# Optimization experiments

Hardware: AMD Instinct MI355X
Metric: run time of the kernel (lower is better)

Reference implementation:

```python
import jax, jax.numpy as jnp
import numpy as np
import math

B, S, E, H, DFF = 8, 1024, 1024, 16, 4096
DK = E // H
EPS = 1e-6


def _layernorm(x, alpha, bias):
    # Faithful to the torch module: uses unbiased std (ddof=1) and divides by (std + eps)
    mean = jnp.mean(x, axis=-1, keepdims=True)
    var = jnp.sum((x - mean) ** 2, axis=-1, keepdims=True) / (x.shape[-1] - 1)
    std = jnp.sqrt(var)
    return alpha * (x - mean) / (std + EPS) + bias


def setup_inputs() -> dict:
    key = jax.random.key(0)
    ks = jax.random.split(key, 16)
    sc_e = 1.0 / math.sqrt(E)
    sc_f = 1.0 / math.sqrt(DFF)
    inp = {
        "x": jax.random.normal(ks[0], (B, S, E), dtype=jnp.float32),
        "mask": jnp.ones((1, 1, S, S), dtype=jnp.int32),
        # linear weights stored as (in, out)
        "wq": jax.random.normal(ks[1], (E, E), jnp.float32) * sc_e,
        "bq": jnp.zeros((E,), jnp.float32),
        "wk": jax.random.normal(ks[2], (E, E), jnp.float32) * sc_e,
        "bk": jnp.zeros((E,), jnp.float32),
        "wv": jax.random.normal(ks[3], (E, E), jnp.float32) * sc_e,
        "bv": jnp.zeros((E,), jnp.float32),
        "wo": jax.random.normal(ks[4], (E, E), jnp.float32) * sc_e,
        "bo": jnp.zeros((E,), jnp.float32),
        "w1": jax.random.normal(ks[5], (E, DFF), jnp.float32) * sc_e,
        "b1": jnp.zeros((DFF,), jnp.float32),
        "w2": jax.random.normal(ks[6], (DFF, E), jnp.float32) * sc_f,
        "b2": jnp.zeros((E,), jnp.float32),
        "ln1_a": jnp.ones((E,), jnp.float32),
        "ln1_b": jnp.zeros((E,), jnp.float32),
        "ln2_a": jnp.ones((E,), jnp.float32),
        "ln2_b": jnp.zeros((E,), jnp.float32),
    }
    return inp


def _mha(x, mask, wq, bq, wk, bk, wv, bv, wo, bo):
    q = (x @ wq + bq).reshape(B, S, H, DK).transpose(0, 2, 1, 3)  # [B,H,S,DK]
    k = (x @ wk + bk).reshape(B, S, H, DK).transpose(0, 2, 1, 3)
    v = (x @ wv + bv).reshape(B, S, H, DK).transpose(0, 2, 1, 3)
    scores = jnp.einsum("bhqd,bhkd->bhqk", q, k) / math.sqrt(DK)  # [B,H,S,S]
    scores = jnp.where(mask == 0, jnp.float32(-1e9), scores)
    attn = jax.nn.softmax(scores, axis=-1)
    out = jnp.einsum("bhqk,bhkd->bhqd", attn, v)  # [B,H,S,DK]
    out = out.transpose(0, 2, 1, 3).reshape(B, S, E)
    return out @ wo + bo


def reference(x, mask, wq, bq, wk, bk, wv, bv, wo, bo, w1, b1, w2, b2,
              ln1_a, ln1_b, ln2_a, ln2_b):
    # Residual connection 1 (pre-norm): x + dropout(attn(norm(x))) ; dropout=0 at eval
    h1 = x + _mha(_layernorm(x, ln1_a, ln1_b), mask, wq, bq, wk, bk, wv, bv, wo, bo)
    # Residual connection 2: h1 + ffn(norm(h1))
    n2 = _layernorm(h1, ln2_a, ln2_b)
    ff = jax.nn.relu(n2 @ w1 + b1) @ w2 + b2
    return h1 + ff
```

## Files before the change

kernel.cpp:

```cpp
#include <hip/hip_runtime.h>
#include <hip/hip_bf16.h>
#include <cstdint>
#include <cstddef>

#define BB   8
#define SS   1024
#define EE   1024
#define HH   16
#define DKK  64
#define DFFN 4096
#define NROWS (BB*SS)

typedef __attribute__((ext_vector_type(8))) short short8;
typedef __attribute__((ext_vector_type(4))) short s16x4;
typedef __attribute__((ext_vector_type(4))) float f32x4;

__device__ __forceinline__ short f2bf(float f) {
  __hip_bfloat16 h = __float2bfloat16(f);
  return __builtin_bit_cast(short, h);
}

__device__ __forceinline__ void gload_lds16(const void* g, void* l) {
  __builtin_amdgcn_global_load_lds((const __attribute__((address_space(1))) void*)g,
                                   (__attribute__((address_space(3))) void*)l, 16, 0, 0);
}

__device__ __forceinline__ f32x4 mfma16(s16x4 a, s16x4 b, f32x4 c) {
#if __has_builtin(__builtin_amdgcn_mfma_f32_16x16x16_bf16)
  return __builtin_amdgcn_mfma_f32_16x16x16_bf16(a, b, c, 0, 0, 0);
#elif __has_builtin(__builtin_amdgcn_mfma_f32_16x16x16bf16_1k)
  return __builtin_amdgcn_mfma_f32_16x16x16bf16_1k(a, b, c, 0, 0, 0);
#else
  f32x4 d = c;
  asm("v_mfma_f32_16x16x16_bf16 %0, %1, %2, %0" : "+v"(d) : "v"(a), "v"(b));
  return d;
#endif
}

__global__ __launch_bounds__(256) void wtrans_kernel(const float* __restrict__ in,
                                                     short* __restrict__ out,
                                                     int R, int C) {
  __shared__ float tile[32][33];
  int c0 = blockIdx.x * 32, r0 = blockIdx.y * 32;
  int tx = threadIdx.x, ty = threadIdx.y;
#pragma unroll
  for (int i = 0; i < 32; i += 8)
    tile[ty + i][tx] = in[(size_t)(r0 + ty + i) * C + (c0 + tx)];
  __syncthreads();
#pragma unroll
  for (int i = 0; i < 32; i += 8)
    out[(size_t)(c0 + ty + i) * R + (r0 + tx)] = f2bf(tile[tx][ty + i]);
}

__global__ __launch_bounds__(256) void ln_kernel(const float* __restrict__ x,
                                                 const float* __restrict__ alpha,
                                                 const float* __restrict__ beta,
                                                 short* __restrict__ out) {
  __shared__ float sbuf[4];
  int row = blockIdx.x;
  int tid = threadIdx.x;
  const float* xr = x + (size_t)row * EE;
  float4 v = reinterpret_cast<const float4*>(xr)[tid];
  float s = v.x + v.y + v.z + v.w;
#pragma unroll
  for (int o = 32; o > 0; o >>= 1) s += __shfl_down(s, o);
  if ((tid & 63) == 0) sbuf[tid >> 6] = s;
  __syncthreads();
  float mean = (sbuf[0] + sbuf[1] + sbuf[2] + sbuf[3]) * (1.0f / EE);
  __syncthreads();
  float dx = v.x - mean, dy = v.y - mean, dz = v.z - mean, dw = v.w - mean;
  float sq = dx * dx + dy * dy + dz * dz + dw * dw;
#pragma unroll
  for (int o = 32; o > 0; o >>= 1) sq += __shfl_down(sq, o);
  if ((tid & 63) == 0) sbuf[tid >> 6] = sq;
  __syncthreads();
  float var = (sbuf[0] + sbuf[1] + sbuf[2] + sbuf[3]) * (1.0f / (EE - 1));
  float inv = 1.0f / (sqrtf(var) + 1e-6f);
  float4 a = reinterpret_cast<const float4*>(alpha)[tid];
  float4 b = reinterpret_cast<const float4*>(beta)[tid];
  size_t base = (size_t)row * EE + tid * 4;
  out[base + 0] = f2bf(a.x * dx * inv + b.x);
  out[base + 1] = f2bf(a.y * dy * inv + b.y);
  out[base + 2] = f2bf(a.z * dz * inv + b.z);
  out[base + 3] = f2bf(a.w * dw * inv + b.w);
}

template <int EPI>
__global__ __launch_bounds__(512, 2) void gemm256(const short* __restrict__ A,
                                                  const short* __restrict__ Bt,
                                                  const float* __restrict__ bias,
                                                  const float* __restrict__ resid,
                                                  void* __restrict__ out,
                                                  int N, int K, int NTN) {
  extern __shared__ char lds[];
  int tid = threadIdx.x, lane = tid & 63, w = tid >> 6;
  int wm = w >> 2, wn = w & 3;
  int g = lane >> 4, c = lane & 15;

  int nwg = gridDim.x, wg = blockIdx.x;
  int swg = (wg & 7) * (nwg >> 3) + (wg >> 3);
  int mt = swg / NTN, nt = swg % NTN;
  int m0 = mt * 256, n0 = nt * 256;

  int rS = tid >> 3;
  int gslot = (tid & 7) ^ ((tid >> 4) & 7);
  const short* pA = A + (size_t)(m0 + rS) * K + gslot * 8;
  const short* pB = Bt + (size_t)(n0 + rS) * K + gslot * 8;

#define STAGE_A(b, h, T)                                                                   \
  {                                                                                        \
    gload_lds16(pA + (size_t)((h)*128) * K + (size_t)(T)*64,                               \
                lds + (b)*32768 + (h)*16384 + tid * 16);                                   \
    gload_lds16(pA + (size_t)((h)*128 + 64) * K + (size_t)(T)*64,                          \
                lds + (b)*32768 + (h)*16384 + 8192 + tid * 16);                            \
  }
#define STAGE_B(b, h, T)                                                                   \
  {                                                                                        \
    gload_lds16(pB + (size_t)((h)*128) * K + (size_t)(T)*64,                               \
                lds + 65536 + (b)*32768 + (h)*16384 + tid * 16);                           \
    gload_lds16(pB + (size_t)((h)*128 + 64) * K + (size_t)(T)*64,                          \
                lds + 65536 + (b)*32768 + (h)*16384 + 8192 + tid * 16);                    \
  }
#define WAITV(NN) asm volatile("s_waitcnt vmcnt(" #NN ")" ::: "memory")

  int aoff0 = ((0 * 4 + g) ^ (c >> 1)) * 16;
  int aoff1 = ((1 * 4 + g) ^ (c >> 1)) * 16;
  char* ldsAb = lds + (wm * 128 + c) * 128;
  char* ldsBb = lds + 65536 + (wn * 64 + c) * 128;

  f32x4 acc[8][4] = {};
  short8 af[2][2], bfr[4][2];

#define READB(b)                                                                           \
  {                                                                                        \
    _Pragma("unroll") for (int nf = 0; nf < 4; ++nf) {                                     \
      bfr[nf][0] = *(const short8*)(ldsBb + (b)*32768 + nf * 2048 + aoff0);                \
      bfr[nf][1] = *(const short8*)(ldsBb + (b)*32768 + nf * 2048 + aoff1);                \
    }                                                                                      \
  }

#define PHASE(b, q, STAGEOP, ENDWAIT)                                                      \
  {                                                                                        \
    _Pragma("unroll") for (int mi = 0; mi < 2; ++mi) {                                     \
      af[mi][0] = *(const short8*)(ldsAb + (b)*32768 + ((q)*32 + mi * 16) * 128 + aoff0);  \
      af[mi][1] = *(const short8*)(ldsAb + (b)*32768 + ((q)*32 + mi * 16) * 128 + aoff1);  \
    }                                                                                      \
    STAGEOP;                                                                               \
    __builtin_amdgcn_s_barrier();                                                          \
    asm volatile("s_waitcnt lgkmcnt(0)" ::: "memory");                                     \
    __builtin_amdgcn_sched_barrier(0);                                                     \
    __builtin_amdgcn_s_setprio(1);                                                         \
    _Pragma("unroll") for (int mi = 0; mi < 2; ++mi)                                       \
      _Pragma("unroll") for (int nf = 0; nf < 4; ++nf) {                                   \
        acc[(q)*2 + mi][nf] = __builtin_amdgcn_mfma_f32_16x16x32_bf16(                     \
            af[mi][0], bfr[nf][0], acc[(q)*2 + mi][nf], 0, 0, 0);                          \
        acc[(q)*2 + mi][nf] = __builtin_amdgcn_mfma_f32_16x16x32_bf16(                     \
            af[mi][1], bfr[nf][1], acc[(q)*2 + mi][nf], 0, 0, 0);                          \
      }                                                                                    \
    __builtin_amdgcn_s_setprio(0);                                                         \
    ENDWAIT;                                                                               \
    __builtin_amdgcn_s_barrier();                                                          \
  }

  int NKT = K >> 6;

  STAGE_A(0, 0, 0); STAGE_A(0, 1, 0);
  STAGE_B(0, 0, 0); STAGE_B(0, 1, 0);
  STAGE_B(1, 0, 1); STAGE_B(1, 1, 1);
  WAITV(4);
  __builtin_amdgcn_s_barrier();

  for (int t = 0; t < NKT - 2; t += 2) {
    READB(0);
    PHASE(0, 0, STAGE_A(1, 0, t + 1), );
    PHASE(0, 1, STAGE_A(1, 1, t + 1), );
    PHASE(0, 2, STAGE_B(0, 0, t + 2), );
    PHASE(0, 3, STAGE_B(0, 1, t + 2), WAITV(4));
    READB(1);
    PHASE(1, 0, STAGE_A(0, 0, t + 2), );
    PHASE(1, 1, STAGE_A(0, 1, t + 2), );
    PHASE(1, 2, STAGE_B(1, 0, t + 3), );
    PHASE(1, 3, STAGE_B(1, 1, t + 3), WAITV(4));
  }
  {
    int t = NKT - 2;
    READB(0);
    PHASE(0, 0, STAGE_A(1, 0, t + 1), );
    PHASE(0, 1, STAGE_A(1, 1, t + 1), );
    PHASE(0, 2, , );
    PHASE(0, 3, , WAITV(0));
    READB(1);
    PHASE(1, 0, , );
    PHASE(1, 1, , );
    PHASE(1, 2, , );
    PHASE(1, 3, , );
  }

#undef STAGE_A
#undef STAGE_B
#undef READB
#undef PHASE
#undef WAITV

  int rb_ = m0 + wm * 128;
  int cb_ = n0 + wn * 64;
#pragma unroll
  for (int fm = 0; fm < 8; ++fm) {
#pragma unroll
    for (int nf = 0; nf < 4; ++nf) {
      int col = cb_ + nf * 16 + c;
      float bv = bias[col];
      if (EPI == 5) {
        int which = col >> 10;
        int inner = col & 1023;
        int h = inner >> 6, d = inner & 63;
        if (which < 2) {
          short* dst = (short*)out + (size_t)which * (8u * 1024 * 1024);
#pragma unroll
          for (int j = 0; j < 4; ++j) {
            int row = rb_ + fm * 16 + g * 4 + j;
            int b = row >> 10, s = row & 1023;
            dst[(((size_t)(b * HH + h)) * SS + s) * DKK + d] = f2bf(acc[fm][nf][j] + bv);
          }
        } else {
          int row0 = rb_ + fm * 16 + g * 4;
          int b = row0 >> 10, s0 = row0 & 1023;
          s16x4 pkv;
#pragma unroll
          for (int j = 0; j < 4; ++j) pkv[j] = f2bf(acc[fm][nf][j] + bv);
          *(s16x4*)((short*)out + 2u * 8 * 1024 * 1024 +
                    (((size_t)(b * HH + h)) * DKK + d) * SS + s0) = pkv;
        }
      } else {
#pragma unroll
        for (int j = 0; j < 4; ++j) {
          int row = rb_ + fm * 16 + g * 4 + j;
          float val = acc[fm][nf][j] + bv;
          if (EPI == 1) {
            ((short*)out)[(size_t)row * N + col] = f2bf(val > 0.f ? val : 0.f);
          } else {
            ((float*)out)[(size_t)row * N + col] = resid[(size_t)row * N + col] + val;
          }
        }
      }
    }
  }
}

__global__ __launch_bounds__(512, 1) void gemm256x128(const short* __restrict__ A,
                                                      const short* __restrict__ Bt,
                                                      const float* __restrict__ bias,
                                                      const float* __restrict__ resid,
                                                      float* __restrict__ out,
                                                      int N, int K, int NTN) {
  extern __shared__ char lds[];
  int tid = threadIdx.x, lane = tid & 63, w = tid >> 6;
  int wm = w >> 1, wn = w & 1;
  int g = lane >> 4, c = lane & 15;

  int nwg = gridDim.x, wg = blockIdx.x;
  int swg = (wg & 7) * (nwg >> 3) + (wg >> 3);
  int mt = swg / NTN, nt = swg % NTN;
  int m0 = mt * 256, n0 = nt * 128;

  int rS = tid >> 3;
  int gslot = (tid & 7) ^ ((tid >> 4) & 7);
  const short* pA = A + (size_t)(m0 + rS) * K + gslot * 8;
  const short* pB = Bt + (size_t)(n0 + rS) * K + gslot * 8;

#define STAGE_A(b, h, T)                                                                   \
  {                                                                                        \
    gload_lds16(pA + (size_t)((h)*128) * K + (size_t)(T)*64,                               \
                lds + (b)*32768 + (h)*16384 + tid * 16);                                   \
    gload_lds16(pA + (size_t)((h)*128 + 64) * K + (size_t)(T)*64,                          \
                lds + (b)*32768 + (h)*16384 + 8192 + tid * 16);                            \
  }
#define STAGE_B(b, T)                                                                      \
  {                                                                                        \
    gload_lds16(pB + (size_t)(T)*64,            lds + 65536 + (b)*16384 + tid * 16);       \
    gload_lds16(pB + (size_t)64 * K + (size_t)(T)*64,                                      \
                lds + 65536 + (b)*16384 + 8192 + tid * 16);                                \
  }
#define WAITV(NN) asm volatile("s_waitcnt vmcnt(" #NN ")" ::: "memory")

  int aoff0 = ((0 * 4 + g) ^ (c >> 1)) * 16;
  int aoff1 = ((1 * 4 + g) ^ (c >> 1)) * 16;
  char* ldsAb = lds + (wm * 64 + c) * 128;
  char* ldsBb = lds + 65536 + (wn * 64 + c) * 128;

  f32x4 acc[4][4] = {};
  short8 af[2][2], bfr[4][2];

#define READB(b)                                                                           \
  {                                                                                        \
    _Pragma("unroll") for (int nf = 0; nf < 4; ++nf) {                                     \
      bfr[nf][0] = *(const short8*)(ldsBb + (b)*16384 + nf * 2048 + aoff0);                \
      bfr[nf][1] = *(const short8*)(ldsBb + (b)*16384 + nf * 2048 + aoff1);                \
    }                                                                                      \
  }

#define PHASE(b, q, STAGEOP, ENDWAIT)                                                      \
  {                                                                                        \
    _Pragma("unroll") for (int mi = 0; mi < 2; ++mi) {                                     \
      af[mi][0] = *(const short8*)(ldsAb + (b)*32768 + ((q)*32 + mi * 16) * 128 + aoff0);  \
      af[mi][1] = *(const short8*)(ldsAb + (b)*32768 + ((q)*32 + mi * 16) * 128 + aoff1);  \
    }                                                                                      \
    STAGEOP;                                                                               \
    __builtin_amdgcn_s_barrier();                                                          \
    asm volatile("s_waitcnt lgkmcnt(0)" ::: "memory");                                     \
    __builtin_amdgcn_sched_barrier(0);                                                     \
    __builtin_amdgcn_s_setprio(1);                                                         \
    _Pragma("unroll") for (int mi = 0; mi < 2; ++mi)                                       \
      _Pragma("unroll") for (int nf = 0; nf < 4; ++nf) {                                   \
        acc[(q)*2 + mi][nf] = __builtin_amdgcn_mfma_f32_16x16x32_bf16(                     \
            af[mi][0], bfr[nf][0], acc[(q)*2 + mi][nf], 0, 0, 0);                          \
        acc[(q)*2 + mi][nf] = __builtin_amdgcn_mfma_f32_16x16x32_bf16(                     \
            af[mi][1], bfr[nf][1], acc[(q)*2 + mi][nf], 0, 0, 0);                          \
      }                                                                                    \
    __builtin_amdgcn_s_setprio(0);                                                         \
    ENDWAIT;                                                                               \
    __builtin_amdgcn_s_barrier();                                                          \
  }

  int NKT = K >> 6;

  STAGE_A(0, 0, 0); STAGE_A(0, 1, 0);
  STAGE_B(0, 0);
  STAGE_B(1, 1);
  WAITV(2);
  __builtin_amdgcn_s_barrier();

  for (int t = 0; t < NKT - 2; t += 2) {
    READB(0);
    PHASE(0, 0, STAGE_A(1, 0, t + 1); STAGE_A(1, 1, t + 1), );
    PHASE(0, 1, STAGE_B(0, t + 2), WAITV(2));
    READB(1);
    PHASE(1, 0, STAGE_A(0, 0, t + 2); STAGE_A(0, 1, t + 2), );
    PHASE(1, 1, STAGE_B(1, t + 3), WAITV(2));
  }
  READB(0);
  PHASE(0, 0, STAGE_A(1, 0, NKT - 1); STAGE_A(1, 1, NKT - 1), );
  PHASE(0, 1, , WAITV(0));
  READB(1);
  PHASE(1, 0, , );
  PHASE(1, 1, , );

#undef STAGE_A
#undef STAGE_B
#undef READB
#undef PHASE
#undef WAITV

  int rb_ = m0 + wm * 64;
  int cb_ = n0 + wn * 64;
#pragma unroll
  for (int fm = 0; fm < 4; ++fm) {
#pragma unroll
    for (int nf = 0; nf < 4; ++nf) {
      int col = cb_ + nf * 16 + c;
      float bv = bias[col];
#pragma unroll
      for (int j = 0; j < 4; ++j) {
        int row = rb_ + fm * 16 + g * 4 + j;
        out[(size_t)row * N + col] = resid[(size_t)row * N + col] + acc[fm][nf][j] + bv;
      }
    }
  }
}

__global__ __launch_bounds__(256, 3) void attn_kernel(const short* __restrict__ q,
                                                      const short* __restrict__ k,
                                                      const short* __restrict__ vt,
                                                      short* __restrict__ out) {
  __shared__ short Ks[2][64 * 64];
  __shared__ short Vs[2][64 * 64];
  int bh = blockIdx.x, qt = blockIdx.y;
  int tid = threadIdx.x, lane = tid & 63, w = tid >> 6;
  int g = lane >> 4, c = lane & 15;
  const short* qp = q + (size_t)bh * SS * DKK;
  const short* kp = k + (size_t)bh * SS * DKK;
  const short* vp = vt + (size_t)bh * DKK * SS;

  int q0 = qt * 128 + w * 32;

  short8 qf[2][2];
#pragma unroll
  for (int qb = 0; qb < 2; ++qb)
#pragma unroll
    for (int ks = 0; ks < 2; ++ks)
      qf[qb][ks] = *(const short8*)(qp + (size_t)(q0 + qb * 16 + c) * DKK + ks * 32 + g * 8);

  f32x4 oacc[2][4];
#pragma unroll
  for (int qb = 0; qb < 2; ++qb)
#pragma unroll
    for (int nd = 0; nd < 4; ++nd)
#pragma unroll
      for (int j = 0; j < 4; ++j) oacc[qb][nd][j] = 0.f;
  float mrun[2] = {-1e30f, -1e30f}, lrun[2] = {0.f, 0.f};

  int rs = lane >> 3;
  int cs = lane & 7;
  int swz = (cs ^ rs) * 8;

  int buf = 0;
#define STAGE(B, T)                                                                  \
  {                                                                                  \
    _Pragma("unroll")                                                                \
    for (int cc = 0; cc < 2; ++cc) {                                                 \
      int chunk = w * 2 + cc;                                                        \
      int row = chunk * 8 + rs;                                                      \
      gload_lds16(kp + (size_t)((T) * 64 + row) * DKK + swz, &Ks[B][chunk * 512]);   \
      gload_lds16(vp + (size_t)row * SS + (T) * 64 + swz, &Vs[B][chunk * 512]);      \
    }                                                                                \
  }

  STAGE(0, 0);
  __syncthreads();

  for (int t = 0; t < SS / 64; ++t) {
    if (t < SS / 64 - 1) STAGE(buf ^ 1, t + 1);

    f32x4 sc[2][4];
#pragma unroll
    for (int qb = 0; qb < 2; ++qb)
#pragma unroll
      for (int nf = 0; nf < 4; ++nf)
#pragma unroll
        for (int j = 0; j < 4; ++j) sc[qb][nf][j] = 0.f;
#pragma unroll
    for (int ks = 0; ks < 2; ++ks) {
      short8 kf[4];
#pragma unroll
      for (int nf = 0; nf < 4; ++nf) {
        int row = nf * 16 + c;
        int off = row * 64 + (((ks * 64 + g * 16) ^ ((c & 7) << 4)) >> 1);
        kf[nf] = *(const short8*)&Ks[buf][off];
      }
#pragma unroll
      for (int qb = 0; qb < 2; ++qb)
#pragma unroll
        for (int nf = 0; nf < 4; ++nf)
          sc[qb][nf] = __builtin_amdgcn_mfma_f32_16x16x32_bf16(kf[nf], qf[qb][ks], sc[qb][nf], 0, 0, 0);
    }

    s16x4 pk[2][4];
    float corr[2];
#pragma unroll
    for (int qb = 0; qb < 2; ++qb) {
      float pm = -1e30f;
#pragma unroll
      for (int nf = 0; nf < 4; ++nf)
#pragma unroll
        for (int j = 0; j < 4; ++j) pm = fmaxf(pm, sc[qb][nf][j]);
      pm = fmaxf(pm, __shfl_xor(pm, 16));
      pm = fmaxf(pm, __shfl_xor(pm, 32));
      pm *= 0.125f;
      float mnew = fmaxf(mrun[qb], pm);
      corr[qb] = __expf(mrun[qb] - mnew);
      mrun[qb] = mnew;
      float rsum = 0.f;
#pragma unroll
      for (int nf = 0; nf < 4; ++nf) {
        float p0 = __expf(sc[qb][nf][0] * 0.125f - mnew);
        float p1 = __expf(sc[qb][nf][1] * 0.125f - mnew);
        float p2 = __expf(sc[qb][nf][2] * 0.125f - mnew);
        float p3 = __expf(sc[qb][nf][3] * 0.125f - mnew);
        rsum += (p0 + p1) + (p2 + p3);
        pk[qb][nf][0] = f2bf(p0); pk[qb][nf][1] = f2bf(p1);
        pk[qb][nf][2] = f2bf(p2); pk[qb][nf][3] = f2bf(p3);
      }
      rsum += __shfl_xor(rsum, 16);
      rsum += __shfl_xor(rsum, 32);
      lrun[qb] = lrun[qb] * corr[qb] + rsum;
    }
#pragma unroll
    for (int qb = 0; qb < 2; ++qb) {
      float cj[4];
#pragma unroll
      for (int j = 0; j < 4; ++j) cj[j] = __shfl(corr[qb], (lane & 48) | (g * 4 + j));
#pragma unroll
      for (int nd = 0; nd < 4; ++nd)
#pragma unroll
        for (int j = 0; j < 4; ++j) oacc[qb][nd][j] *= cj[j];
    }

#pragma unroll
    for (int nf = 0; nf < 4; ++nf) {
      s16x4 vf[4];
#pragma unroll
      for (int nd = 0; nd < 4; ++nd) {
        int row = nd * 16 + c;
        int off = row * 64 + (((nf * 32 + g * 8) ^ ((c & 7) << 4)) >> 1);
        vf[nd] = *(const s16x4*)&Vs[buf][off];
      }
#pragma unroll
      for (int qb = 0; qb < 2; ++qb)
#pragma unroll
        for (int nd = 0; nd < 4; ++nd)
          oacc[qb][nd] = mfma16(pk[qb][nf], vf[nd], oacc[qb][nd]);
    }
    __syncthreads();
    buf ^= 1;
  }
#undef STAGE

  int b = bh >> 4, h = bh & 15;
#pragma unroll
  for (int qb = 0; qb < 2; ++qb) {
#pragma unroll
    for (int j = 0; j < 4; ++j) {
      float linv = 1.0f / __shfl(lrun[qb], (lane & 48) | (g * 4 + j));
      int srow = q0 + qb * 16 + g * 4 + j;
#pragma unroll
      for (int nd = 0; nd < 4; ++nd)
        out[((size_t)b * SS + srow) * EE + h * DKK + nd * 16 + c] = f2bf(oacc[qb][nd][j] * linv);
    }
  }
}

extern "C" void kernel_launch(void* const* d_in, const int* in_sizes, int n_in,
                              void* d_out, int out_size, void* d_ws, size_t ws_size,
                              hipStream_t stream) {
  (void)in_sizes; (void)n_in; (void)out_size; (void)ws_size;
  const float* x   = (const float*)d_in[0];
  const float* wq  = (const float*)d_in[2];  const float* bq  = (const float*)d_in[3];
  const float* wk  = (const float*)d_in[4];  const float* bk  = (const float*)d_in[5];
  const float* wv  = (const float*)d_in[6];  const float* bv  = (const float*)d_in[7];
  const float* wo  = (const float*)d_in[8];  const float* bo  = (const float*)d_in[9];
  const float* w1  = (const float*)d_in[10]; const float* b1  = (const float*)d_in[11];
  const float* w2  = (const float*)d_in[12]; const float* b2  = (const float*)d_in[13];
  const float* l1a = (const float*)d_in[14]; const float* l1b = (const float*)d_in[15];
  const float* l2a = (const float*)d_in[16]; const float* l2b = (const float*)d_in[17];
  float* out = (float*)d_out;

  char* ws = (char*)d_ws;
  const size_t MB = 1024ull * 1024ull;
  short* wqkvT = (short*)(ws + 0 * MB);
  short* woT = (short*)(ws + 6 * MB);
  short* w1T = (short*)(ws + 8 * MB);
  short* w2T = (short*)(ws + 16 * MB);
  short* n1  = (short*)(ws + 24 * MB);
  short* qb  = (short*)(ws + 40 * MB);
  short* ff1 = (short*)(ws + 40 * MB);
  short* ao  = (short*)(ws + 88 * MB);
  float* bqkv = (float*)(ws + 100 * MB);
  float* h1  = (float*)(ws + 104 * MB);

  hipMemcpyAsync(bqkv,        bq, EE * sizeof(float), hipMemcpyDeviceToDevice, stream);
  hipMemcpyAsync(bqkv + EE,   bk, EE * sizeof(float), hipMemcpyDeviceToDevice, stream);
  hipMemcpyAsync(bqkv + 2*EE, bv, EE * sizeof(float), hipMemcpyDeviceToDevice, stream);

  dim3 tb(32, 8);
  wtrans_kernel<<<dim3(EE / 32, EE / 32), tb, 0, stream>>>(wq, wqkvT, EE, EE);
  wtrans_kernel<<<dim3(EE / 32, EE / 32), tb, 0, stream>>>(wk, wqkvT + 1024 * 1024, EE, EE);
  wtrans_kernel<<<dim3(EE / 32, EE / 32), tb, 0, stream>>>(wv, wqkvT + 2 * 1024 * 1024, EE, EE);
  wtrans_kernel<<<dim3(EE / 32, EE / 32), tb, 0, stream>>>(wo, woT, EE, EE);
  wtrans_kernel<<<dim3(DFFN / 32, EE / 32), tb, 0, stream>>>(w1, w1T, EE, DFFN);
  wtrans_kernel<<<dim3(EE / 32, DFFN / 32), tb, 0, stream>>>(w2, w2T, DFFN, EE);

  ln_kernel<<<NROWS, 256, 0, stream>>>(x, l1a, l1b, n1);

  gemm256<5><<<dim3(32 * 12), 512, 131072, stream>>>(n1, wqkvT, bqkv, nullptr, qb, 3072, EE, 12);

  attn_kernel<<<dim3(BB * HH, SS / 128), 256, 0, stream>>>(qb, qb + 8 * 1024 * 1024,
                                                           qb + 16 * 1024 * 1024, ao);

  gemm256x128<<<dim3(256), 512, 98304, stream>>>(ao, woT, bo, x, h1, EE, EE, 8);

  ln_kernel<<<NROWS, 256, 0, stream>>>(h1, l2a, l2b, n1);

  gemm256<1><<<dim3(32 * 16), 512, 131072, stream>>>(n1, w1T, b1, nullptr, ff1, DFFN, EE, 16);
  gemm256x128<<<dim3(256), 512, 98304, stream>>>(ff1, w2T, b2, h1, out, EE, DFFN, 8);
}
```

Baseline: 374.3 us.

## Fold softmax scale into Q, use exp2 with lazy rescale and MFMA priority

The Q projection epilogue now multiplies Q by log2(e)/sqrt(dk), so the attention loop can call exp2 directly without per-element scaling. The online softmax skips the running-max update and the output-accumulator rescale whenever the new tile maximum stays within 8 (log2 units) of the running max, a check made wave-wide with __all. s_setprio raises wave priority around the MFMA blocks so matrix work from different waves interleaves with the softmax math. The lazy-max path lets exponents reach up to 2^8 before rescaling, which slightly changes bf16 rounding of P, and the two divergent branches add code size.

```diff
diff --git a/kernel.cpp b/kernel.cpp
--- a/kernel.cpp
+++ b/kernel.cpp
@@ -10,6 +10,8 @@
 #define DKK  64
 #define DFFN 4096
 #define NROWS (BB*SS)
+
+#define QSCALE 0.18033688011112042f
 
 typedef __attribute__((ext_vector_type(8))) short short8;
 typedef __attribute__((ext_vector_type(4))) short s16x4;
@@ -220,7 +222,9 @@
           for (int j = 0; j < 4; ++j) {
             int row = rb_ + fm * 16 + g * 4 + j;
             int b = row >> 10, s = row & 1023;
-            dst[(((size_t)(b * HH + h)) * SS + s) * DKK + d] = f2bf(acc[fm][nf][j] + bv);
+            float val = acc[fm][nf][j] + bv;
+            if (which == 0) val *= QSCALE;
+            dst[(((size_t)(b * HH + h)) * SS + s) * DKK + d] = f2bf(val);
           }
         } else {
           int row0 = rb_ + fm * 16 + g * 4;
@@ -428,6 +432,7 @@
       for (int nf = 0; nf < 4; ++nf)
 #pragma unroll
         for (int j = 0; j < 4; ++j) sc[qb][nf][j] = 0.f;
+    __builtin_amdgcn_s_setprio(1);
 #pragma unroll
     for (int ks = 0; ks < 2; ++ks) {
       short8 kf[4];
@@ -443,9 +448,9 @@
         for (int nf = 0; nf < 4; ++nf)
           sc[qb][nf] = __builtin_amdgcn_mfma_f32_16x16x32_bf16(kf[nf], qf[qb][ks], sc[qb][nf], 0, 0, 0);
     }
+    __builtin_amdgcn_s_setprio(0);
 
     s16x4 pk[2][4];
-    float corr[2];
 #pragma unroll
     for (int qb = 0; qb < 2; ++qb) {
       float pm = -1e30f;
@@ -455,36 +460,51 @@
         for (int j = 0; j < 4; ++j) pm = fmaxf(pm, sc[qb][nf][j]);
       pm = fmaxf(pm, __shfl_xor(pm, 16));
       pm = fmaxf(pm, __shfl_xor(pm, 32));
-      pm *= 0.125f;
-      float mnew = fmaxf(mrun[qb], pm);
-      corr[qb] = __expf(mrun[qb] - mnew);
-      mrun[qb] = mnew;
-      float rsum = 0.f;
-#pragma unroll
-      for (int nf = 0; nf < 4; ++nf) {
-        float p0 = __expf(sc[qb][nf][0] * 0.125f - mnew);
-        float p1 = __expf(sc[qb][nf][1] * 0.125f - mnew);
-        float p2 = __expf(sc[qb][nf][2] * 0.125f - mnew);
-        float p3 = __expf(sc[qb][nf][3] * 0.125f - mnew);
-        rsum += (p0 + p1) + (p2 + p3);
-        pk[qb][nf][0] = f2bf(p0); pk[qb][nf][1] = f2bf(p1);
-        pk[qb][nf][2] = f2bf(p2); pk[qb][nf][3] = f2bf(p3);
+      float mcur = mrun[qb];
+      if (__all(pm <= mcur + 8.0f)) {
+        float rsum = 0.f;
+#pragma unroll
+        for (int nf = 0; nf < 4; ++nf) {
+          float p0 = exp2f(sc[qb][nf][0] - mcur);
+          float p1 = exp2f(sc[qb][nf][1] - mcur);
+          float p2 = exp2f(sc[qb][nf][2] - mcur);
+          float p3 = exp2f(sc[qb][nf][3] - mcur);
+          rsum += (p0 + p1) + (p2 + p3);
+          pk[qb][nf][0] = f2bf(p0); pk[qb][nf][1] = f2bf(p1);
+          pk[qb][nf][2] = f2bf(p2); pk[qb][nf][3] = f2bf(p3);
+        }
+        rsum += __shfl_xor(rsum, 16);
+        rsum += __shfl_xor(rsum, 32);
+        lrun[qb] += rsum;
+      } else {
+        float mnew = fmaxf(mcur, pm);
+        float corr = exp2f(mcur - mnew);
+        mrun[qb] = mnew;
+        float rsum = 0.f;
+#pragma unroll
+        for (int nf = 0; nf < 4; ++nf) {
+          float p0 = exp2f(sc[qb][nf][0] - mnew);
+          float p1 = exp2f(sc[qb][nf][1] - mnew);
+          float p2 = exp2f(sc[qb][nf][2] - mnew);
+          float p3 = exp2f(sc[qb][nf][3] - mnew);
+          rsum += (p0 + p1) + (p2 + p3);
+          pk[qb][nf][0] = f2bf(p0); pk[qb][nf][1] = f2bf(p1);
+          pk[qb][nf][2] = f2bf(p2); pk[qb][nf][3] = f2bf(p3);
+        }
+        rsum += __shfl_xor(rsum, 16);
+        rsum += __shfl_xor(rsum, 32);
+        lrun[qb] = lrun[qb] * corr + rsum;
+        float cj[4];
+#pragma unroll
+        for (int j = 0; j < 4; ++j) cj[j] = __shfl(corr, (lane & 48) | (g * 4 + j));
+#pragma unroll
+        for (int nd = 0; nd < 4; ++nd)
+#pragma unroll
+          for (int j = 0; j < 4; ++j) oacc[qb][nd][j] *= cj[j];
       }
-      rsum += __shfl_xor(rsum, 16);
-      rsum += __shfl_xor(rsum, 32);
-      lrun[qb] = lrun[qb] * corr[qb] + rsum;
     }
-#pragma unroll
-    for (int qb = 0; qb < 2; ++qb) {
-      float cj[4];
-#pragma unroll
-      for (int j = 0; j < 4; ++j) cj[j] = __shfl(corr[qb], (lane & 48) | (g * 4 + j));
-#pragma unroll
-      for (int nd = 0; nd < 4; ++nd)
-#pragma unroll
-        for (int j = 0; j < 4; ++j) oacc[qb][nd][j] *= cj[j];
-    }
-
+
+    __builtin_amdgcn_s_setprio(1);
 #pragma unroll
     for (int nf = 0; nf < 4; ++nf) {
       s16x4 vf[4];
@@ -500,6 +520,7 @@
         for (int nd = 0; nd < 4; ++nd)
           oacc[qb][nd] = mfma16(pk[qb][nf], vf[nd], oacc[qb][nd]);
     }
+    __builtin_amdgcn_s_setprio(0);
     __syncthreads();
     buf ^= 1;
   }
```

Measured after the change: 381.2 us. Within noise of the previous version (+1.8%).
